# Kernel tuning notes

Measured on AMD Instinct MI355X. Metric: run time of the kernel, lower is better.

## Reference

```python
import jax, jax.numpy as jnp
import numpy as np

ALPHA = 3.5
BETA = 0.5
GAMMA = 0.5
LAM = 0.5


def setup_inputs() -> dict:
    key = jax.random.key(0)
    k1, k2 = jax.random.split(key)
    b, c, t = 32, 512, 4096
    x = jax.random.normal(k1, (b, c, t), dtype=jnp.float32)
    # original: z0 ~ U[0.25, 0.75]
    z0 = jax.random.uniform(k2, (b, c), dtype=jnp.float32) * 0.5 + 0.25
    return {"x": x, "z0": z0}


def reference(x, z0):
    # x: (b, c, t), z0: (b, c)
    x_t_first = jnp.transpose(x, (2, 0, 1))  # (t, b, c)

    def step(z, x_t):
        sigma_in = ALPHA * z * (1.0 - z) + BETA * x_t
        z_next = (1.0 - GAMMA) * z + GAMMA * 0.5 * (1.0 + jnp.tanh(sigma_in))
        z_next = jnp.clip(z_next, 0.0, 1.0)
        u_t = LAM * x_t + (1.0 - LAM) * (2.0 * z_next - 1.0)
        return z_next, u_t

    _, u = jax.lax.scan(step, z0, x_t_first)  # u: (t, b, c)
    return jnp.transpose(u, (1, 2, 0))  # (b, c, t)
```

## Files before the change

### kernel.cpp

```cpp
#include <hip/hip_runtime.h>


#define SEQ_T   4096
#define CHUNK   256
#define NCHUNK  16
#define NSTAGE  8
#define SEQ_PB  16
#define NPIECE  256

__device__ __forceinline__ void chaos_step(float& z, float xs, float& us) {
    const float CA = -10.098865286222744f;
    const float CB = -1.4426950408889634f;
    float p  = CB * xs;
    float hz = 0.5f * z;
    float zz = __builtin_fmaf(-z, z, z);
    float s  = __builtin_fmaf(CA, zz, p);
    float e  = exp2f(s);
    float r  = __builtin_amdgcn_rcpf(e + 1.0f);
    z = __builtin_fmaf(0.5f, r, hz);
    us = __builtin_fmaf(0.5f, xs, z - 0.5f);
}

__global__ __launch_bounds__(256, 2)
void ChaosModulator_28922309771717_kernel(const float* __restrict__ x,
                                          const float* __restrict__ z0,
                                          float* __restrict__ u) {
    __shared__ float4 lds[2][NPIECE * 8];

    const int tid  = threadIdx.x;
    const int lane = tid & 63;
    const int wid  = tid >> 6;
    const int q4   = lane & 7;
    const int pr   = lane >> 3;
    const int qx   = q4 ^ pr;
    const int myx  = tid & 7;

    const size_t blk_elem = (size_t)blockIdx.x * SEQ_PB * SEQ_T;
    const float4* __restrict__ xb = (const float4*)(x + blk_elem);
    float4*       __restrict__ ub = (float4*)(u + blk_elem);

    int o4[8];
    int sl[8];
#pragma unroll
    for (int j = 0; j < 8; ++j) {
        int p = wid * 64 + j * 8 + pr;
        o4[j] = (p >> 4) * (SEQ_T / 4) + (p & 15) * (CHUNK / 4) + q4;
        sl[j] = p * 8 + qx;
    }

    float4 g[8];

#pragma unroll
    for (int j = 0; j < 8; ++j) g[j] = xb[o4[j] + 6 * 8];
#pragma unroll
    for (int j = 0; j < 8; ++j) lds[0][sl[j]] = g[j];
#pragma unroll
    for (int j = 0; j < 8; ++j) g[j] = xb[o4[j] + 7 * 8];
#pragma unroll
    for (int j = 0; j < 8; ++j) lds[1][sl[j]] = g[j];
    __syncthreads();

    float z = 0.5f;
    {
        const int pn = (tid == 0) ? 0 : tid - 1;
        const int nx = pn & 7;
        float du;
#pragma unroll
        for (int q = 0; q < 8; ++q) {
            float4 w = lds[0][pn * 8 + (q ^ nx)];
            chaos_step(z, w.x, du); chaos_step(z, w.y, du);
            chaos_step(z, w.z, du); chaos_step(z, w.w, du);
        }
#pragma unroll
        for (int q = 0; q < 8; ++q) {
            float4 w = lds[1][pn * 8 + (q ^ nx)];
            chaos_step(z, w.x, du); chaos_step(z, w.y, du);
            chaos_step(z, w.z, du); chaos_step(z, w.w, du);
        }
    }
    if ((tid & 15) == 0) z = z0[blockIdx.x * SEQ_PB + (tid >> 4)];
    __syncthreads();

#pragma unroll
    for (int j = 0; j < 8; ++j) g[j] = xb[o4[j]];
#pragma unroll
    for (int j = 0; j < 8; ++j) lds[0][sl[j]] = g[j];
    __syncthreads();

    for (int s = 0; s < NSTAGE; ++s) {
        float4* cur = lds[s & 1];
        float4* nxt = lds[(s + 1) & 1];

        if (s + 1 < NSTAGE) {
#pragma unroll
            for (int j = 0; j < 8; ++j) g[j] = xb[o4[j] + (s + 1) * 8];
        }

#pragma unroll
        for (int q = 0; q < 8; ++q) {
            const int slot = tid * 8 + (q ^ myx);
            float4 xv = cur[slot];
            float4 uq;
            chaos_step(z, xv.x, uq.x); chaos_step(z, xv.y, uq.y);
            chaos_step(z, xv.z, uq.z); chaos_step(z, xv.w, uq.w);
            cur[slot] = uq;
        }
        __syncthreads();

        if (s + 1 < NSTAGE) {
#pragma unroll
            for (int j = 0; j < 8; ++j) nxt[sl[j]] = g[j];
        }
#pragma unroll
        for (int j = 0; j < 8; ++j) ub[o4[j] + s * 8] = cur[sl[j]];

        __syncthreads();
    }
}

extern "C" void kernel_launch(void* const* d_in, const int* in_sizes, int n_in,
                              void* d_out, int out_size, void* d_ws, size_t ws_size,
                              hipStream_t stream) {
    const float* x  = (const float*)d_in[0];
    const float* z0 = (const float*)d_in[1];
    float* u = (float*)d_out;

    const int n_seq = in_sizes[1];
    dim3 grid(n_seq / SEQ_PB), block(NPIECE);
    ChaosModulator_28922309771717_kernel<<<grid, block, 0, stream>>>(x, z0, u);
}
```

Baseline: 481.8 us.

## Halve stage width, double stages, raise occupancy, use nontemporal stores

Each stage now covers 16 time steps per chunk (4 float4) instead of 32, with 16 stages, and the warm-up loads four stages in two rounds. This halves LDS and register use so launch bounds can request 4 blocks per SM for more latency hiding. The LDS layout switches from an XOR swizzle to a transposed [q][piece] layout, and output writes become nontemporal stores. The cost is twice as many stage barriers and a serialized warm-up with an extra sync.

```diff
diff --git a/kernel.cpp b/kernel.cpp
--- a/kernel.cpp
+++ b/kernel.cpp
@@ -3,10 +3,12 @@
 
 #define SEQ_T   4096
 #define CHUNK   256
-#define NCHUNK  16
-#define NSTAGE  8
+#define NSTAGE  16
+#define WF4     4
 #define SEQ_PB  16
 #define NPIECE  256
+
+typedef float fx4 __attribute__((ext_vector_type(4)));
 
 __device__ __forceinline__ void chaos_step(float& z, float xs, float& us) {
     const float CA = -10.098865286222744f;
@@ -21,59 +23,72 @@
     us = __builtin_fmaf(0.5f, xs, z - 0.5f);
 }
 
-__global__ __launch_bounds__(256, 2)
+__global__ __launch_bounds__(256, 4)
 void ChaosModulator_28922309771717_kernel(const float* __restrict__ x,
                                           const float* __restrict__ z0,
                                           float* __restrict__ u) {
-    __shared__ float4 lds[2][NPIECE * 8];
+    __shared__ float4 lds[2][NPIECE * WF4];
 
     const int tid  = threadIdx.x;
     const int lane = tid & 63;
     const int wid  = tid >> 6;
-    const int q4   = lane & 7;
-    const int pr   = lane >> 3;
-    const int qx   = q4 ^ pr;
-    const int myx  = tid & 7;
+    const int q4   = lane & 3;
+    const int pr   = lane >> 2;
 
     const size_t blk_elem = (size_t)blockIdx.x * SEQ_PB * SEQ_T;
     const float4* __restrict__ xb = (const float4*)(x + blk_elem);
-    float4*       __restrict__ ub = (float4*)(u + blk_elem);
+    fx4*          __restrict__ ub = (fx4*)(u + blk_elem);
 
-    int o4[8];
-    int sl[8];
+    int o4[WF4];
+    int sl[WF4];
 #pragma unroll
-    for (int j = 0; j < 8; ++j) {
-        int p = wid * 64 + j * 8 + pr;
+    for (int j = 0; j < WF4; ++j) {
+        int p = wid * 64 + j * 16 + pr;
         o4[j] = (p >> 4) * (SEQ_T / 4) + (p & 15) * (CHUNK / 4) + q4;
-        sl[j] = p * 8 + qx;
+        sl[j] = q4 * NPIECE + p;
     }
 
-    float4 g[8];
+    float4 g[WF4];
 
 #pragma unroll
-    for (int j = 0; j < 8; ++j) g[j] = xb[o4[j] + 6 * 8];
+    for (int j = 0; j < WF4; ++j) g[j] = xb[o4[j] + 12 * WF4];
 #pragma unroll
-    for (int j = 0; j < 8; ++j) lds[0][sl[j]] = g[j];
+    for (int j = 0; j < WF4; ++j) lds[0][sl[j]] = g[j];
 #pragma unroll
-    for (int j = 0; j < 8; ++j) g[j] = xb[o4[j] + 7 * 8];
+    for (int j = 0; j < WF4; ++j) g[j] = xb[o4[j] + 13 * WF4];
 #pragma unroll
-    for (int j = 0; j < 8; ++j) lds[1][sl[j]] = g[j];
+    for (int j = 0; j < WF4; ++j) lds[1][sl[j]] = g[j];
     __syncthreads();
 
     float z = 0.5f;
-    {
-        const int pn = (tid == 0) ? 0 : tid - 1;
-        const int nx = pn & 7;
-        float du;
+    const int pn = (tid == 0) ? 0 : tid - 1;
+    float du;
 #pragma unroll
-        for (int q = 0; q < 8; ++q) {
-            float4 w = lds[0][pn * 8 + (q ^ nx)];
+    for (int b = 0; b < 2; ++b) {
+#pragma unroll
+        for (int q = 0; q < WF4; ++q) {
+            float4 w = lds[b][q * NPIECE + pn];
             chaos_step(z, w.x, du); chaos_step(z, w.y, du);
             chaos_step(z, w.z, du); chaos_step(z, w.w, du);
         }
+    }
+    __syncthreads();
+
 #pragma unroll
-        for (int q = 0; q < 8; ++q) {
-            float4 w = lds[1][pn * 8 + (q ^ nx)];
+    for (int j = 0; j < WF4; ++j) g[j] = xb[o4[j] + 14 * WF4];
+#pragma unroll
+    for (int j = 0; j < WF4; ++j) lds[0][sl[j]] = g[j];
+#pragma unroll
+    for (int j = 0; j < WF4; ++j) g[j] = xb[o4[j] + 15 * WF4];
+#pragma unroll
+    for (int j = 0; j < WF4; ++j) lds[1][sl[j]] = g[j];
+    __syncthreads();
+
+#pragma unroll
+    for (int b = 0; b < 2; ++b) {
+#pragma unroll
+        for (int q = 0; q < WF4; ++q) {
+            float4 w = lds[b][q * NPIECE + pn];
             chaos_step(z, w.x, du); chaos_step(z, w.y, du);
             chaos_step(z, w.z, du); chaos_step(z, w.w, du);
         }
@@ -82,9 +97,9 @@
     __syncthreads();
 
 #pragma unroll
-    for (int j = 0; j < 8; ++j) g[j] = xb[o4[j]];
+    for (int j = 0; j < WF4; ++j) g[j] = xb[o4[j]];
 #pragma unroll
-    for (int j = 0; j < 8; ++j) lds[0][sl[j]] = g[j];
+    for (int j = 0; j < WF4; ++j) lds[0][sl[j]] = g[j];
     __syncthreads();
 
     for (int s = 0; s < NSTAGE; ++s) {
@@ -93,12 +108,12 @@
 
         if (s + 1 < NSTAGE) {
 #pragma unroll
-            for (int j = 0; j < 8; ++j) g[j] = xb[o4[j] + (s + 1) * 8];
+            for (int j = 0; j < WF4; ++j) g[j] = xb[o4[j] + (s + 1) * WF4];
         }
 
 #pragma unroll
-        for (int q = 0; q < 8; ++q) {
-            const int slot = tid * 8 + (q ^ myx);
+        for (int q = 0; q < WF4; ++q) {
+            const int slot = q * NPIECE + tid;
             float4 xv = cur[slot];
             float4 uq;
             chaos_step(z, xv.x, uq.x); chaos_step(z, xv.y, uq.y);
@@ -109,10 +124,14 @@
 
         if (s + 1 < NSTAGE) {
 #pragma unroll
-            for (int j = 0; j < 8; ++j) nxt[sl[j]] = g[j];
+            for (int j = 0; j < WF4; ++j) nxt[sl[j]] = g[j];
         }
 #pragma unroll
-        for (int j = 0; j < 8; ++j) ub[o4[j] + s * 8] = cur[sl[j]];
+        for (int j = 0; j < WF4; ++j) {
+            float4 uq = cur[sl[j]];
+            fx4 uv = { uq.x, uq.y, uq.z, uq.w };
+            __builtin_nontemporal_store(uv, &ub[o4[j] + s * WF4]);
+        }
 
         __syncthreads();
     }
```

Result: slower. 499.6 us (+3.7%).
